# Optimization experiments

Measured on AMD Instinct MI355X. Metric: run time of the kernel, lower is better.

The kernel has to match this reference:

```python
import jax, jax.numpy as jnp
import numpy as np

B, H, W, C = 32, 56, 56, 512
WS, SHIFT, NH = 7, 3, 16
N = WS * WS
NW = (H // WS) * (W // WS)
HID = 4 * C
EPS = 1e-5


def _np_constants():
    # log-spaced relative coords table (SwinV2 CPB input), pretrained_window_size=[0,0]
    rh = np.arange(-(WS - 1), WS, dtype=np.float32)
    tbl = np.stack(np.meshgrid(rh, rh, indexing='ij'), axis=-1)  # (2*WS-1, 2*WS-1, 2)
    tbl = tbl / (WS - 1) * 8.0
    tbl = np.sign(tbl) * np.log2(np.abs(tbl) + 1.0) / np.log2(8.0)
    coords = np.stack(np.meshgrid(np.arange(WS), np.arange(WS), indexing='ij'))
    cf = coords.reshape(2, -1)
    rc = (cf[:, :, None] - cf[:, None, :]).transpose(1, 2, 0).copy()  # (N,N,2)
    rc[..., 0] += WS - 1
    rc[..., 1] += WS - 1
    rc[..., 0] *= 2 * WS - 1
    rpi = rc.sum(-1)  # (N,N) indices into the (2*WS-1)^2 table
    # shifted-window attention mask
    img = np.zeros((H, W), dtype=np.float32)
    sl = (slice(0, -WS), slice(-WS, -SHIFT), slice(-SHIFT, None))
    cnt = 0
    for hs in sl:
        for ws in sl:
            img[hs, ws] = cnt
            cnt += 1
    mw = img.reshape(H // WS, WS, W // WS, WS).transpose(0, 2, 1, 3).reshape(-1, N)
    am = mw[:, None, :] - mw[:, :, None]
    attn_mask = np.where(am != 0, -100.0, 0.0).astype(np.float32)  # (NW,N,N)
    return tbl.reshape(-1, 2).astype(np.float32), rpi.reshape(-1), attn_mask

TBL_NP, RPI_NP, MASK_NP = _np_constants()


def _ln(x, g, b):
    mu = jnp.mean(x, -1, keepdims=True)
    var = jnp.mean((x - mu) ** 2, -1, keepdims=True)
    return (x - mu) * jax.lax.rsqrt(var + EPS) * g + b


def _win_part(x):  # (B,H,W,C) -> (B*NW, N, C)
    x = x.reshape(B, H // WS, WS, W // WS, WS, C).transpose(0, 1, 3, 2, 4, 5)
    return x.reshape(-1, N, C)


def _win_rev(w):  # (B*NW, N, C) -> (B,H,W,C)
    x = w.reshape(B, H // WS, W // WS, WS, WS, C).transpose(0, 1, 3, 2, 4, 5)
    return x.reshape(B, H, W, C)


def setup_inputs() -> dict:
    key = jax.random.key(0)
    ks = jax.random.split(key, 8)
    s = 0.02
    return {
        'x': jax.random.normal(ks[0], (B, H * W, C), jnp.float32),
        'qkv_w': jax.random.normal(ks[1], (3 * C, C), jnp.float32) * s,
        'q_bias': jnp.zeros((C,), jnp.float32),
        'v_bias': jnp.zeros((C,), jnp.float32),
        'logit_scale': jnp.log(10.0) * jnp.ones((NH, 1, 1), jnp.float32),
        'cpb_w1': jax.random.normal(ks[2], (512, 2), jnp.float32) * s,
        'cpb_b1': jnp.zeros((512,), jnp.float32),
        'cpb_w2': jax.random.normal(ks[3], (NH, 512), jnp.float32) * s,
        'proj_w': jax.random.normal(ks[4], (C, C), jnp.float32) * s,
        'proj_b': jnp.zeros((C,), jnp.float32),
        'norm1_g': jnp.ones((C,), jnp.float32),
        'norm1_b': jnp.zeros((C,), jnp.float32),
        'fc1_w': jax.random.normal(ks[5], (HID, C), jnp.float32) * s,
        'fc1_b': jnp.zeros((HID,), jnp.float32),
        'fc2_w': jax.random.normal(ks[6], (C, HID), jnp.float32) * s,
        'fc2_b': jnp.zeros((C,), jnp.float32),
        'norm2_g': jnp.ones((C,), jnp.float32),
        'norm2_b': jnp.zeros((C,), jnp.float32),
    }


def reference(x, qkv_w, q_bias, v_bias, logit_scale, cpb_w1, cpb_b1, cpb_w2,
              proj_w, proj_b, norm1_g, norm1_b, fc1_w, fc1_b, fc2_w, fc2_b,
              norm2_g, norm2_b):
    tbl = jnp.asarray(TBL_NP)
    mask = jnp.asarray(MASK_NP)
    shortcut = x
    xi = x.reshape(B, H, W, C)
    xi = jnp.roll(xi, shift=(-SHIFT, -SHIFT), axis=(1, 2))
    xw = _win_part(xi)  # (B*NW, N, C)
    qkv_bias = jnp.concatenate([q_bias, jnp.zeros_like(v_bias), v_bias])
    qkv = xw @ qkv_w.T + qkv_bias
    qkv = qkv.reshape(-1, N, 3, NH, C // NH).transpose(2, 0, 3, 1, 4)
    q, k, v = qkv[0], qkv[1], qkv[2]  # (B_, NH, N, hd)
    qn = q / jnp.maximum(jnp.linalg.norm(q, axis=-1, keepdims=True), 1e-12)
    kn = k / jnp.maximum(jnp.linalg.norm(k, axis=-1, keepdims=True), 1e-12)
    scale = jnp.exp(jnp.minimum(logit_scale, jnp.log(100.0)))  # (NH,1,1)
    attn = jnp.einsum('bhnd,bhmd->bhnm', qn, kn) * scale
    # CPB MLP -> relative position bias
    hcb = jax.nn.relu(tbl @ cpb_w1.T + cpb_b1)       # (169, 512)
    bias_tbl = hcb @ cpb_w2.T                        # (169, NH)
    rpb = bias_tbl[RPI_NP].reshape(N, N, NH).transpose(2, 0, 1)
    rpb = 16.0 * jax.nn.sigmoid(rpb)
    attn = attn + rpb[None]
    attn = attn.reshape(B, NW, NH, N, N) + mask[None, :, None]
    attn = jax.nn.softmax(attn.reshape(-1, NH, N, N), axis=-1)
    out = jnp.einsum('bhnm,bhmd->bhnd', attn, v).transpose(0, 2, 1, 3).reshape(-1, N, C)
    out = out @ proj_w.T + proj_b
    xi = _win_rev(out)
    xi = jnp.roll(xi, shift=(SHIFT, SHIFT), axis=(1, 2)).reshape(B, H * W, C)
    x = shortcut + _ln(xi, norm1_g, norm1_b)  # SwinV2 post-norm residual
    hmlp = jax.nn.gelu(x @ fc1_w.T + fc1_b, approximate=False)
    m = hmlp @ fc2_w.T + fc2_b
    x = x + _ln(m, norm2_g, norm2_b)
    return x
```

## Files before the change

kernel.cpp:

```cpp
#include <hip/hip_runtime.h>

typedef unsigned short u16;
typedef unsigned int   u32;

using f32x4  = __attribute__((ext_vector_type(4))) float;
using bf16x8 = __attribute__((ext_vector_type(8))) short;

__device__ __forceinline__ float bf2f(u16 u){
  union { u32 i; float f; } x; x.i = ((u32)u) << 16; return x.f;
}
__device__ __forceinline__ u16 f2bf(float f){
  union { float f; u32 i; } x; x.f = f;
  u32 r = x.i + 0x7FFFu + ((x.i >> 16) & 1u);
  return (u16)(r >> 16);
}
__device__ __forceinline__ float gelu_f(float v){
  float u = 0.7978845608f * v * (1.f + 0.044715f*v*v);
  float e = __expf(2.f*u);
  return 0.5f*v*(2.f - 2.f/(e + 1.f));
}

__device__ __forceinline__ void glds16(const void* g, void* l){
  __builtin_amdgcn_global_load_lds(
      (const __attribute__((address_space(1))) unsigned int*)g,
      (__attribute__((address_space(3))) unsigned int*)(unsigned int)(unsigned long long)l,
      16, 0, 0);
}

__device__ __forceinline__ int rollmap(int m){
  int win = m / 49, n = m % 49;
  int b  = win >> 6, wi = win & 63;
  int wh = wi >> 3, ww = wi & 7;
  int r = n / 7, c = n % 7;
  int sh = wh*7 + r + 3; if (sh >= 56) sh -= 56;
  int sw = ww*7 + c + 3; if (sw >= 56) sw -= 56;
  return b*3136 + sh*56 + sw;
}

template<int EPI, int AMODE, int NKT>
__global__ __launch_bounds__(512, 2) void gemm_bt(const u16* __restrict__ A,
      const u16* __restrict__ Bw, const float* __restrict__ bias,
      void* __restrict__ outp, int M, int N, int nbn)
{
  constexpr int K = NKT * 64;
  __shared__ __align__(16) char LDS[2*65536];
  const int t    = threadIdx.x;
  const int lane = t & 63, wave = t >> 6;
  const int wr = wave >> 2, wn = wave & 3;
  const int lr = lane & 15, lk = lane >> 4;

  const int gl = ((blockIdx.x & 7) * ((int)gridDim.x >> 3)) + (blockIdx.x >> 3);
  const int bm = gl / nbn, bn = gl - bm*nbn;

  const int q   = (t & 7) ^ ((t >> 3) & 7);
  const int sr0 = 2*(t >> 3) + (q >> 2);
  const int sch = (q & 3) * 8;
  const u16 *pA0, *pA1;
  if constexpr (AMODE == 0){
    pA0 = A + (size_t)(bm*256 + sr0      )*K + sch;
    pA1 = A + (size_t)(bm*256 + sr0 + 128)*K + sch;
  } else {
    pA0 = A + (size_t)rollmap(bm*256 + sr0      )*K + sch;
    pA1 = A + (size_t)rollmap(bm*256 + sr0 + 128)*K + sch;
  }
  const u16* pB0 = Bw + (size_t)(bn*256 + sr0      )*K + sch;
  const u16* pB1 = Bw + (size_t)(bn*256 + sr0 + 128)*K + sch;

  int oA[8], oB[4];
#pragma unroll
  for (int i = 0; i < 8; ++i){
    int r = wr*128 + i*16 + lr;
    oA[i] = ((r>>1)<<7) + (((((r&1)<<2)|lk) ^ ((r>>1)&7))<<4);
  }
#pragma unroll
  for (int j = 0; j < 4; ++j){
    int r = wn*64 + j*16 + lr;
    oB[j] = ((r>>1)<<7) + (((((r&1)<<2)|lk) ^ ((r>>1)&7))<<4);
  }

  f32x4 acc[8][4];
#pragma unroll
  for (int i = 0; i < 8; ++i)
#pragma unroll
    for (int j = 0; j < 4; ++j) acc[i][j] = (f32x4){0.f, 0.f, 0.f, 0.f};

  auto stgA = [&](int T, int ks, int buf){
    char* d = LDS + buf*65536 + ks*16384 + wave*1024;
    const int e = T*64 + ks*32;
    glds16(pA0 + e, d);
    glds16(pA1 + e, d + 8192);
  };
  auto stgB = [&](int T, int ks, int buf){
    char* d = LDS + buf*65536 + 32768 + ks*16384 + wave*1024;
    const int e = T*64 + ks*32;
    glds16(pB0 + e, d);
    glds16(pB1 + e, d + 8192);
  };

  stgA(0,0,0); stgA(0,1,0); stgB(0,0,0); stgB(0,1,0);
  stgA(1,0,1); stgA(1,1,1); stgB(1,0,1); stgB(1,1,1);
  asm volatile("s_waitcnt vmcnt(8)" ::: "memory");
  __builtin_amdgcn_s_barrier();
  asm volatile("" ::: "memory");

  auto TILE = [&](int T, int buf){
    const char* ld = LDS + buf*65536;
    const bool stP0  = (T >= 1) && (T+1 < NKT);
    const bool st123 = (T+2 < NKT);
    bf16x8 fa[4], fb[4];

#pragma unroll
    for (int j = 0; j < 4; ++j) fb[j] = *(const bf16x8*)(ld + 32768 + oB[j]);
#pragma unroll
    for (int i = 0; i < 4; ++i) fa[i] = *(const bf16x8*)(ld + oA[i]);
    if (stP0) stgA(T+1, 1, buf^1);
    __builtin_amdgcn_s_barrier();
    asm volatile("s_waitcnt lgkmcnt(0)" ::: "memory");
    __builtin_amdgcn_sched_barrier(0);
    __builtin_amdgcn_s_setprio(1);
#pragma unroll
    for (int i = 0; i < 4; ++i)
#pragma unroll
      for (int j = 0; j < 4; ++j)
        acc[i][j] = __builtin_amdgcn_mfma_f32_16x16x32_bf16(fa[i], fb[j], acc[i][j], 0, 0, 0);
    __builtin_amdgcn_s_setprio(0);
    __builtin_amdgcn_s_barrier();
    asm volatile("" ::: "memory");

#pragma unroll
    for (int i = 0; i < 4; ++i) fa[i] = *(const bf16x8*)(ld + oA[4+i]);
    if (st123) stgB(T+2, 0, buf);
    __builtin_amdgcn_s_barrier();
    asm volatile("s_waitcnt lgkmcnt(0)" ::: "memory");
    __builtin_amdgcn_sched_barrier(0);
    __builtin_amdgcn_s_setprio(1);
#pragma unroll
    for (int i = 0; i < 4; ++i)
#pragma unroll
      for (int j = 0; j < 4; ++j)
        acc[4+i][j] = __builtin_amdgcn_mfma_f32_16x16x32_bf16(fa[i], fb[j], acc[4+i][j], 0, 0, 0);
    __builtin_amdgcn_s_setprio(0);
    __builtin_amdgcn_s_barrier();
    asm volatile("" ::: "memory");

#pragma unroll
    for (int j = 0; j < 4; ++j) fb[j] = *(const bf16x8*)(ld + 49152 + oB[j]);
#pragma unroll
    for (int i = 0; i < 4; ++i) fa[i] = *(const bf16x8*)(ld + 16384 + oA[i]);
    if (st123) stgA(T+2, 0, buf);
    __builtin_amdgcn_s_barrier();
    asm volatile("s_waitcnt lgkmcnt(0)" ::: "memory");
    __builtin_amdgcn_sched_barrier(0);
    __builtin_amdgcn_s_setprio(1);
#pragma unroll
    for (int i = 0; i < 4; ++i)
#pragma unroll
      for (int j = 0; j < 4; ++j)
        acc[i][j] = __builtin_amdgcn_mfma_f32_16x16x32_bf16(fa[i], fb[j], acc[i][j], 0, 0, 0);
    __builtin_amdgcn_s_setprio(0);
    __builtin_amdgcn_s_barrier();
    asm volatile("" ::: "memory");

#pragma unroll
    for (int i = 0; i < 4; ++i) fa[i] = *(const bf16x8*)(ld + 16384 + oA[4+i]);
    if (st123) stgB(T+2, 1, buf);
    __builtin_amdgcn_s_barrier();
    asm volatile("s_waitcnt lgkmcnt(0)" ::: "memory");
    __builtin_amdgcn_sched_barrier(0);
    __builtin_amdgcn_s_setprio(1);
#pragma unroll
    for (int i = 0; i < 4; ++i)
#pragma unroll
      for (int j = 0; j < 4; ++j)
        acc[4+i][j] = __builtin_amdgcn_mfma_f32_16x16x32_bf16(fa[i], fb[j], acc[4+i][j], 0, 0, 0);
    __builtin_amdgcn_s_setprio(0);
    if (T <= NKT-3)      asm volatile("s_waitcnt vmcnt(6)" ::: "memory");
    else if (T == NKT-2) asm volatile("s_waitcnt vmcnt(0)" ::: "memory");
    if (T < NKT-1){
      __builtin_amdgcn_s_barrier();
      asm volatile("" ::: "memory");
    }
  };

  for (int p = 0; p < NKT/2; ++p){
    TILE(2*p,     0);
    TILE(2*p + 1, 1);
  }

  const int lc = lane & 15, lg = lane >> 4;
#pragma unroll
  for (int i = 0; i < 8; ++i){
#pragma unroll
    for (int j = 0; j < 4; ++j){
      int cm = bm*256 + wr*128 + i*16 + lg*4;
      int cn = bn*256 + wn*64  + j*16 + lc;
      float bv = bias[cn];
#pragma unroll
      for (int r = 0; r < 4; ++r){
        float v = acc[i][j][r] + bv;
        if (EPI == 2) v = gelu_f(v);
        ((u16*)outp)[(size_t)(cm + r)*N + cn] = f2bf(v);
      }
    }
  }
}

__global__ __launch_bounds__(256, 2) void attn_mfma(const u16* __restrict__ qkv,
      const float* __restrict__ rpb, const float* __restrict__ ls,
      u16* __restrict__ outp)
{
  __shared__ __align__(16) u16 Pl[4][64*72];
  __shared__ __align__(16) u16 Vl[4][32*72];
  __shared__ unsigned char regid[64];
  const int tid  = threadIdx.x, lane = tid & 63, wave = tid >> 6;
  const int lc = lane & 15, lg = lane >> 4;
  const int pair = blockIdx.x*4 + wave;
  const int win = pair >> 4, h = pair & 15;

  const u16* qb = qkv + (size_t)win*49*1536 + h*32;
  const u16* kb = qb + 512;
  const u16* vb = qb + 1024;

  if (tid < 49){
    int wi = win & 63, wh = wi >> 3, ww = wi & 7;
    int q7 = (tid*37) >> 8, r7 = tid - q7*7;
    int gh = wh*7 + q7, gw = ww*7 + r7;
    int rh = gh < 49 ? 0 : (gh < 53 ? 1 : 2);
    int rw = gw < 49 ? 0 : (gw < 53 ? 1 : 2);
    regid[tid] = (unsigned char)(rh*3 + rw);
  }

  u16* V = &Vl[wave][0];
#pragma unroll
  for (int it = 0; it < 4; ++it){
    int ch = it*64 + lane;
    int n = ch >> 2, oct = ch & 3;
    union { int4 i4; u16 s[8]; } v8;
    if (n < 49) v8.i4 = *(const int4*)(vb + (size_t)n*1536 + oct*8);
    else        v8.i4 = make_int4(0,0,0,0);
#pragma unroll
    for (int q = 0; q < 8; ++q) V[(oct*8 + q)*72 + n] = v8.s[q];
  }

  const float scale = __expf(fminf(ls[h], 4.6051702f));
  bf16x8 qf[4], kf[4];
#pragma unroll
  for (int ti = 0; ti < 4; ++ti){
    const int n = ti*16 + lc;
    {
      union { int4 i4; u16 s[8]; } raw;
      raw.i4 = *(const int4*)(qb + (size_t)n*1536 + lg*8);
      float f[8]; float ss = 0.f;
#pragma unroll
      for (int q = 0; q < 8; ++q){ f[q] = bf2f(raw.s[q]); ss += f[q]*f[q]; }
      ss += __shfl_xor(ss, 16); ss += __shfl_xor(ss, 32);
      const float inv = scale / fmaxf(sqrtf(ss), 1e-12f);
      union { short s[8]; bf16x8 v; } o;
#pragma unroll
      for (int q = 0; q < 8; ++q) o.s[q] = (short)f2bf(f[q]*inv);
      qf[ti] = o.v;
    }
    {
      union { int4 i4; u16 s[8]; } raw;
      raw.i4 = *(const int4*)(kb + (size_t)n*1536 + lg*8);
      float f[8]; float ss = 0.f;
#pragma unroll
      for (int q = 0; q < 8; ++q){ f[q] = bf2f(raw.s[q]); ss += f[q]*f[q]; }
      ss += __shfl_xor(ss, 16); ss += __shfl_xor(ss, 32);
      const float inv = 1.f / fmaxf(sqrtf(ss), 1e-12f);
      union { short s[8]; bf16x8 v; } o;
#pragma unroll
      for (int q = 0; q < 8; ++q) o.s[q] = (short)f2bf(f[q]*inv);
      kf[ti] = o.v;
    }
  }
  __syncthreads();

  f32x4 acc[4][4];
#pragma unroll
  for (int i = 0; i < 4; ++i)
#pragma unroll
    for (int j = 0; j < 4; ++j) acc[i][j] = (f32x4){0.f,0.f,0.f,0.f};
#pragma unroll
  for (int i = 0; i < 4; ++i)
#pragma unroll
    for (int j = 0; j < 4; ++j)
      acc[i][j] = __builtin_amdgcn_mfma_f32_16x16x32_bf16(qf[i], kf[j], acc[i][j], 0, 0, 0);

  u16* P = &Pl[wave][0];
  int rj[4];
#pragma unroll
  for (int tj = 0; tj < 4; ++tj){
    int j = tj*16 + lc;
    rj[tj] = (int)regid[j < 49 ? j : 0];
  }
  const float* rpbh = rpb + h*2401;
#pragma unroll
  for (int ti = 0; ti < 4; ++ti){
#pragma unroll
    for (int r = 0; r < 4; ++r){
      const int i = ti*16 + lg*4 + r;
      const bool iv = i < 49;
      const int ic = iv ? i : 0;
      const int ri = (int)regid[ic];
      const float* rrow = rpbh + ic*49;
      float sv[4];
#pragma unroll
      for (int tj = 0; tj < 4; ++tj){
        const int j = tj*16 + lc;
        float t2 = acc[ti][tj][r] + rrow[j < 49 ? j : 0];
        if (ri != rj[tj]) t2 -= 100.f;
        sv[tj] = (iv && j < 49) ? t2 : -1e30f;
      }
      float mx = fmaxf(fmaxf(sv[0],sv[1]), fmaxf(sv[2],sv[3]));
      mx = fmaxf(mx, __shfl_xor(mx, 1));
      mx = fmaxf(mx, __shfl_xor(mx, 2));
      mx = fmaxf(mx, __shfl_xor(mx, 4));
      mx = fmaxf(mx, __shfl_xor(mx, 8));
      float p[4], sum = 0.f;
#pragma unroll
      for (int tj = 0; tj < 4; ++tj){ p[tj] = __expf(sv[tj] - mx); sum += p[tj]; }
      sum += __shfl_xor(sum, 1); sum += __shfl_xor(sum, 2);
      sum += __shfl_xor(sum, 4); sum += __shfl_xor(sum, 8);
      const float rs = __builtin_amdgcn_rcpf(sum);
#pragma unroll
      for (int tj = 0; tj < 4; ++tj) P[i*72 + tj*16 + lc] = f2bf(p[tj]*rs);
    }
  }
  __syncthreads();

  f32x4 o[4][2];
#pragma unroll
  for (int i = 0; i < 4; ++i){ o[i][0] = (f32x4){0.f,0.f,0.f,0.f}; o[i][1] = (f32x4){0.f,0.f,0.f,0.f}; }
#pragma unroll
  for (int ks = 0; ks < 2; ++ks){
    bf16x8 pa[4], vf[2];
#pragma unroll
    for (int ti = 0; ti < 4; ++ti)
      pa[ti] = *(const bf16x8*)((const char*)P + (ti*16 + lc)*144 + (ks*4 + lg)*16);
#pragma unroll
    for (int tc = 0; tc < 2; ++tc)
      vf[tc] = *(const bf16x8*)((const char*)V + (tc*16 + lc)*144 + (ks*4 + lg)*16);
#pragma unroll
    for (int ti = 0; ti < 4; ++ti)
#pragma unroll
      for (int tc = 0; tc < 2; ++tc)
        o[ti][tc] = __builtin_amdgcn_mfma_f32_16x16x32_bf16(pa[ti], vf[tc], o[ti][tc], 0, 0, 0);
  }

#pragma unroll
  for (int ti = 0; ti < 4; ++ti){
#pragma unroll
    for (int tc = 0; tc < 2; ++tc){
#pragma unroll
      for (int r = 0; r < 4; ++r){
        const int i = ti*16 + lg*4 + r;
        if (i < 49)
          outp[((size_t)win*49 + i)*512 + h*32 + tc*16 + lc] = f2bf(o[ti][tc][r]);
      }
    }
  }
}

__global__ __launch_bounds__(256) void ln1_kernel(const u16* __restrict__ xb,
      const u16* __restrict__ y, const float* __restrict__ g, const float* __restrict__ bt,
      float* __restrict__ xout, u16* __restrict__ xbf)
{
  __shared__ float red[8];
  const int t = blockIdx.x;
  const int b = t / 3136, s = t % 3136;
  const int hh = s / 56, ww2 = s % 56;
  int ph = hh + 53; if (ph >= 56) ph -= 56;
  int pw = ww2 + 53; if (pw >= 56) pw -= 56;
  const int win = b*64 + (ph/7)*8 + (pw/7);
  const int n   = (ph%7)*7 + (pw%7);
  const u16* yr = y + ((size_t)win*49 + n)*512;
  const int c = threadIdx.x * 2;
  u32 u = *(const u32*)(yr + c);
  float vx = bf2f((u16)(u & 0xffff)), vy = bf2f((u16)(u >> 16));
  float sum = vx + vy, sq = vx*vx + vy*vy;
#pragma unroll
  for (int off = 32; off; off >>= 1){ sum += __shfl_xor(sum, off); sq += __shfl_xor(sq, off); }
  if ((threadIdx.x & 63) == 0){ red[threadIdx.x >> 6] = sum; red[(threadIdx.x >> 6) + 4] = sq; }
  __syncthreads();
  sum = red[0]+red[1]+red[2]+red[3];
  sq  = red[4]+red[5]+red[6]+red[7];
  const float mu  = sum * (1.f/512.f);
  const float inv = rsqrtf(fmaxf(sq * (1.f/512.f) - mu*mu, 0.f) + 1e-5f);
  u32 ux = *(const u32*)(xb + (size_t)t*512 + c);
  float o0 = bf2f((u16)(ux & 0xffff)) + (vx - mu)*inv*g[c]   + bt[c];
  float o1 = bf2f((u16)(ux >> 16))    + (vy - mu)*inv*g[c+1] + bt[c+1];
  float* orow = xout + (size_t)t*512;
  orow[c] = o0; orow[c+1] = o1;
  *(u32*)(xbf + (size_t)t*512 + c) = (u32)f2bf(o0) | ((u32)f2bf(o1) << 16);
}

__global__ __launch_bounds__(256) void ln2_kernel(const u16* __restrict__ m,
      const float* __restrict__ g, const float* __restrict__ bt, float* __restrict__ out)
{
  __shared__ float red[8];
  const int t = blockIdx.x;
  const int c = threadIdx.x * 2;
  u32 u = *(const u32*)(m + (size_t)t*512 + c);
  float v0 = bf2f((u16)(u & 0xffff)), v1 = bf2f((u16)(u >> 16));
  float sum = v0 + v1, sq = v0*v0 + v1*v1;
#pragma unroll
  for (int off = 32; off; off >>= 1){ sum += __shfl_xor(sum, off); sq += __shfl_xor(sq, off); }
  if ((threadIdx.x & 63) == 0){ red[threadIdx.x >> 6] = sum; red[(threadIdx.x >> 6) + 4] = sq; }
  __syncthreads();
  sum = red[0]+red[1]+red[2]+red[3];
  sq  = red[4]+red[5]+red[6]+red[7];
  const float mu  = sum * (1.f/512.f);
  const float inv = rsqrtf(fmaxf(sq * (1.f/512.f) - mu*mu, 0.f) + 1e-5f);
  float* orow = out + (size_t)t*512;
  orow[c]   += (v0 - mu)*inv*g[c]   + bt[c];
  orow[c+1] += (v1 - mu)*inv*g[c+1] + bt[c+1];
}

__global__ void cast_bf16_kernel(const float* __restrict__ in, u16* __restrict__ out, int n4){
  int i = blockIdx.x*256 + threadIdx.x;
  if (i >= n4) return;
  float4 v = *(const float4*)(in + (size_t)i*4);
  u32 lo = (u32)f2bf(v.x) | ((u32)f2bf(v.y) << 16);
  u32 hi = (u32)f2bf(v.z) | ((u32)f2bf(v.w) << 16);
  *(uint2*)(out + (size_t)i*4) = make_uint2(lo, hi);
}
__global__ void qkvbias_kernel(const float* __restrict__ qb, const float* __restrict__ vb,
                               float* __restrict__ out){
  int i = blockIdx.x*256 + threadIdx.x;
  if (i >= 1536) return;
  out[i] = i < 512 ? qb[i] : (i < 1024 ? 0.f : vb[i - 1024]);
}
__device__ __forceinline__ float cpb_coord(int d){
  float v = (float)(d - 6) * (8.f/6.f);
  float m = log2f(fabsf(v) + 1.f) * (1.f/3.f);
  return v > 0.f ? m : (v < 0.f ? -m : 0.f);
}
__global__ void cpb_kernel(const float* __restrict__ w1, const float* __restrict__ b1,
                           const float* __restrict__ w2, float* __restrict__ btbl){
  int idx = blockIdx.x*256 + threadIdx.x;
  if (idx >= 169*16) return;
  int e = idx >> 4, h = idx & 15;
  float t0 = cpb_coord(e / 13), t1 = cpb_coord(e % 13);
  float acc = 0.f;
  for (int jj = 0; jj < 512; ++jj){
    float hid = fmaxf(t0*w1[jj*2] + t1*w1[jj*2+1] + b1[jj], 0.f);
    acc += hid * w2[h*512 + jj];
  }
  btbl[e*16 + h] = acc;
}
__global__ void rpb_kernel(const float* __restrict__ btbl, float* __restrict__ rpb){
  int idx = blockIdx.x*256 + threadIdx.x;
  if (idx >= 16*49*49) return;
  int hh = idx / 2401, ij = idx % 2401, i = ij / 49, j = ij % 49;
  int dr = i/7 - j/7 + 6, dc = i%7 - j%7 + 6;
  float bb = btbl[(dr*13 + dc)*16 + hh];
  rpb[idx] = 16.f / (1.f + __expf(-bb));
}

extern "C" void kernel_launch(void* const* d_in, const int* in_sizes, int n_in,
                              void* d_out, int out_size, void* d_ws, size_t ws_size,
                              hipStream_t stream)
{
  const float* x    = (const float*)d_in[0];
  const float* qkvw = (const float*)d_in[1];
  const float* qb   = (const float*)d_in[2];
  const float* vb   = (const float*)d_in[3];
  const float* ls   = (const float*)d_in[4];
  const float* cw1  = (const float*)d_in[5];
  const float* cb1  = (const float*)d_in[6];
  const float* cw2  = (const float*)d_in[7];
  const float* pw   = (const float*)d_in[8];
  const float* pb   = (const float*)d_in[9];
  const float* n1g  = (const float*)d_in[10];
  const float* n1b  = (const float*)d_in[11];
  const float* f1w  = (const float*)d_in[12];
  const float* f1b  = (const float*)d_in[13];
  const float* f2w  = (const float*)d_in[14];
  const float* f2b  = (const float*)d_in[15];
  const float* n2g  = (const float*)d_in[16];
  const float* n2b  = (const float*)d_in[17];

  char* ws = (char*)d_ws;
  const size_t SZ_BIG = (size_t)100352 * 2048 * 2;
  const size_t SZ_MID = (size_t)100352 * 512  * 2;
  size_t o = SZ_BIG + SZ_MID;
  u16* wqkv  = (u16*)(ws + o); o += (size_t)1536*512*2;
  u16* wproj = (u16*)(ws + o); o += (size_t)512*512*2;
  u16* wfc1  = (u16*)(ws + o); o += (size_t)2048*512*2;
  u16* wfc2  = (u16*)(ws + o); o += (size_t)512*2048*2;
  float* qkvbias = (float*)(ws + o); o += 1536*4;
  float* btbl    = (float*)(ws + o); o += 2704*4;
  float* rpb     = (float*)(ws + o); o += 38416*4;

  u16*   xbf   = (u16*)ws;
  u16*   qkvo  = (u16*)(ws + (size_t)100352*512*2);
  u16*   y_h   = qkvo;
  u16*   big_h = (u16*)ws;
  u16*   mid   = (u16*)(ws + SZ_BIG);
  float* out   = (float*)d_out;

  cast_bf16_kernel<<<768,  256, 0, stream>>>(qkvw, wqkv, 1536*512/4);
  cast_bf16_kernel<<<256,  256, 0, stream>>>(pw,  wproj, 512*512/4);
  cast_bf16_kernel<<<1024, 256, 0, stream>>>(f1w, wfc1, 2048*512/4);
  cast_bf16_kernel<<<1024, 256, 0, stream>>>(f2w, wfc2, 512*2048/4);
  qkvbias_kernel<<<6, 256, 0, stream>>>(qb, vb, qkvbias);
  cpb_kernel<<<11, 256, 0, stream>>>(cw1, cb1, cw2, btbl);
  rpb_kernel<<<151, 256, 0, stream>>>(btbl, rpb);
  cast_bf16_kernel<<<50176, 256, 0, stream>>>(x, xbf, 100352*512/4);

  gemm_bt<0,2,8><<<392*6, 512, 0, stream>>>(xbf, wqkv, qkvbias,
                                            (void*)qkvo, 100352, 1536, 6);
  attn_mfma<<<8192, 256, 0, stream>>>(qkvo, rpb, ls, mid);
  gemm_bt<0,0,8><<<392*2, 512, 0, stream>>>(mid, wproj, pb,
                                            (void*)y_h, 100352, 512, 2);
  ln1_kernel<<<100352, 256, 0, stream>>>(xbf, y_h, n1g, n1b, out, mid);
  gemm_bt<2,0,8><<<392*8, 512, 0, stream>>>(mid, wfc1, f1b,
                                            (void*)big_h, 100352, 2048, 8);
  gemm_bt<0,0,32><<<392*2, 512, 0, stream>>>(big_h, wfc2, f2b,
                                             (void*)mid, 100352, 512, 2);
  ln2_kernel<<<100352, 256, 0, stream>>>(mid, n2g, n2b, out);
}
```

Baseline: 1.454 ms.

## Shrink GEMM K-tile to 32 with simple double-buffered loop

Restructures the bf16 GEMM main loop so each step processes a 32-wide K slab instead of a 64-wide tile split into two half-stages. It uses a plain two-buffer ping-pong that prefetches only the next slab, and drops the vmcnt(6) deep-prefetch scheme along with most intra-tile barriers. LDS drops to 64 KB, which could raise occupancy, and the launch-bounds hint for two blocks per CU is removed. In exchange the loop now waits on vmcnt(0) every iteration, so each slab's global load latency is less well hidden.

Result: slower. 1.525 ms (median of 3 runs) (+4.9%).

```diff
diff --git a/kernel.cpp b/kernel.cpp
--- a/kernel.cpp
+++ b/kernel.cpp
@@ -38,12 +38,12 @@
 }
 
 template<int EPI, int AMODE, int NKT>
-__global__ __launch_bounds__(512, 2) void gemm_bt(const u16* __restrict__ A,
+__global__ __launch_bounds__(512) void gemm_bt(const u16* __restrict__ A,
       const u16* __restrict__ Bw, const float* __restrict__ bias,
       void* __restrict__ outp, int M, int N, int nbn)
 {
-  constexpr int K = NKT * 64;
-  __shared__ __align__(16) char LDS[2*65536];
+  constexpr int K = NKT * 32;
+  __shared__ __align__(16) char LDS[2*32768];
   const int t    = threadIdx.x;
   const int lane = t & 63, wave = t >> 6;
   const int wr = wave >> 2, wn = wave & 3;
@@ -84,37 +84,34 @@
 #pragma unroll
     for (int j = 0; j < 4; ++j) acc[i][j] = (f32x4){0.f, 0.f, 0.f, 0.f};
 
-  auto stgA = [&](int T, int ks, int buf){
-    char* d = LDS + buf*65536 + ks*16384 + wave*1024;
-    const int e = T*64 + ks*32;
+  auto stgA = [&](int T, int buf){
+    char* d = LDS + buf*32768 + wave*1024;
+    const int e = T*32;
     glds16(pA0 + e, d);
     glds16(pA1 + e, d + 8192);
   };
-  auto stgB = [&](int T, int ks, int buf){
-    char* d = LDS + buf*65536 + 32768 + ks*16384 + wave*1024;
-    const int e = T*64 + ks*32;
+  auto stgB = [&](int T, int buf){
+    char* d = LDS + buf*32768 + 16384 + wave*1024;
+    const int e = T*32;
     glds16(pB0 + e, d);
     glds16(pB1 + e, d + 8192);
   };
 
-  stgA(0,0,0); stgA(0,1,0); stgB(0,0,0); stgB(0,1,0);
-  stgA(1,0,1); stgA(1,1,1); stgB(1,0,1); stgB(1,1,1);
-  asm volatile("s_waitcnt vmcnt(8)" ::: "memory");
+  stgA(0, 0); stgB(0, 0);
+  asm volatile("s_waitcnt vmcnt(0)" ::: "memory");
   __builtin_amdgcn_s_barrier();
   asm volatile("" ::: "memory");
 
-  auto TILE = [&](int T, int buf){
-    const char* ld = LDS + buf*65536;
-    const bool stP0  = (T >= 1) && (T+1 < NKT);
-    const bool st123 = (T+2 < NKT);
+  for (int T = 0; T < NKT; ++T){
+    const char* ld = LDS + (T & 1)*32768;
+    const int nb = (T & 1) ^ 1;
     bf16x8 fa[4], fb[4];
 
-#pragma unroll
-    for (int j = 0; j < 4; ++j) fb[j] = *(const bf16x8*)(ld + 32768 + oB[j]);
+    if (T + 1 < NKT) stgA(T + 1, nb);
+#pragma unroll
+    for (int j = 0; j < 4; ++j) fb[j] = *(const bf16x8*)(ld + 16384 + oB[j]);
 #pragma unroll
     for (int i = 0; i < 4; ++i) fa[i] = *(const bf16x8*)(ld + oA[i]);
-    if (stP0) stgA(T+1, 1, buf^1);
-    __builtin_amdgcn_s_barrier();
     asm volatile("s_waitcnt lgkmcnt(0)" ::: "memory");
     __builtin_amdgcn_sched_barrier(0);
     __builtin_amdgcn_s_setprio(1);
@@ -124,13 +121,10 @@
       for (int j = 0; j < 4; ++j)
         acc[i][j] = __builtin_amdgcn_mfma_f32_16x16x32_bf16(fa[i], fb[j], acc[i][j], 0, 0, 0);
     __builtin_amdgcn_s_setprio(0);
-    __builtin_amdgcn_s_barrier();
-    asm volatile("" ::: "memory");
-
+
+    if (T + 1 < NKT) stgB(T + 1, nb);
 #pragma unroll
     for (int i = 0; i < 4; ++i) fa[i] = *(const bf16x8*)(ld + oA[4+i]);
-    if (st123) stgB(T+2, 0, buf);
-    __builtin_amdgcn_s_barrier();
     asm volatile("s_waitcnt lgkmcnt(0)" ::: "memory");
     __builtin_amdgcn_sched_barrier(0);
     __builtin_amdgcn_s_setprio(1);
@@ -140,51 +134,12 @@
       for (int j = 0; j < 4; ++j)
         acc[4+i][j] = __builtin_amdgcn_mfma_f32_16x16x32_bf16(fa[i], fb[j], acc[4+i][j], 0, 0, 0);
     __builtin_amdgcn_s_setprio(0);
-    __builtin_amdgcn_s_barrier();
-    asm volatile("" ::: "memory");
-
-#pragma unroll
-    for (int j = 0; j < 4; ++j) fb[j] = *(const bf16x8*)(ld + 49152 + oB[j]);
-#pragma unroll
-    for (int i = 0; i < 4; ++i) fa[i] = *(const bf16x8*)(ld + 16384 + oA[i]);
-    if (st123) stgA(T+2, 0, buf);
-    __builtin_amdgcn_s_barrier();
-    asm volatile("s_waitcnt lgkmcnt(0)" ::: "memory");
-    __builtin_amdgcn_sched_barrier(0);
-    __builtin_amdgcn_s_setprio(1);
-#pragma unroll
-    for (int i = 0; i < 4; ++i)
-#pragma unroll
-      for (int j = 0; j < 4; ++j)
-        acc[i][j] = __builtin_amdgcn_mfma_f32_16x16x32_bf16(fa[i], fb[j], acc[i][j], 0, 0, 0);
-    __builtin_amdgcn_s_setprio(0);
-    __builtin_amdgcn_s_barrier();
-    asm volatile("" ::: "memory");
-
-#pragma unroll
-    for (int i = 0; i < 4; ++i) fa[i] = *(const bf16x8*)(ld + 16384 + oA[4+i]);
-    if (st123) stgB(T+2, 1, buf);
-    __builtin_amdgcn_s_barrier();
-    asm volatile("s_waitcnt lgkmcnt(0)" ::: "memory");
-    __builtin_amdgcn_sched_barrier(0);
-    __builtin_amdgcn_s_setprio(1);
-#pragma unroll
-    for (int i = 0; i < 4; ++i)
-#pragma unroll
-      for (int j = 0; j < 4; ++j)
-        acc[4+i][j] = __builtin_amdgcn_mfma_f32_16x16x32_bf16(fa[i], fb[j], acc[4+i][j], 0, 0, 0);
-    __builtin_amdgcn_s_setprio(0);
-    if (T <= NKT-3)      asm volatile("s_waitcnt vmcnt(6)" ::: "memory");
-    else if (T == NKT-2) asm volatile("s_waitcnt vmcnt(0)" ::: "memory");
-    if (T < NKT-1){
+
+    if (T + 1 < NKT){
+      asm volatile("s_waitcnt vmcnt(0)" ::: "memory");
       __builtin_amdgcn_s_barrier();
       asm volatile("" ::: "memory");
     }
-  };
-
-  for (int p = 0; p < NKT/2; ++p){
-    TILE(2*p,     0);
-    TILE(2*p + 1, 1);
   }
 
   const int lc = lane & 15, lg = lane >> 4;
@@ -509,15 +464,15 @@
   rpb_kernel<<<151, 256, 0, stream>>>(btbl, rpb);
   cast_bf16_kernel<<<50176, 256, 0, stream>>>(x, xbf, 100352*512/4);
 
-  gemm_bt<0,2,8><<<392*6, 512, 0, stream>>>(xbf, wqkv, qkvbias,
-                                            (void*)qkvo, 100352, 1536, 6);
+  gemm_bt<0,2,16><<<392*6, 512, 0, stream>>>(xbf, wqkv, qkvbias,
+                                             (void*)qkvo, 100352, 1536, 6);
   attn_mfma<<<8192, 256, 0, stream>>>(qkvo, rpb, ls, mid);
-  gemm_bt<0,0,8><<<392*2, 512, 0, stream>>>(mid, wproj, pb,
-                                            (void*)y_h, 100352, 512, 2);
+  gemm_bt<0,0,16><<<392*2, 512, 0, stream>>>(mid, wproj, pb,
+                                             (void*)y_h, 100352, 512, 2);
   ln1_kernel<<<100352, 256, 0, stream>>>(xbf, y_h, n1g, n1b, out, mid);
-  gemm_bt<2,0,8><<<392*8, 512, 0, stream>>>(mid, wfc1, f1b,
-                                            (void*)big_h, 100352, 2048, 8);
-  gemm_bt<0,0,32><<<392*2, 512, 0, stream>>>(big_h, wfc2, f2b,
+  gemm_bt<2,0,16><<<392*8, 512, 0, stream>>>(mid, wfc1, f1b,
+                                             (void*)big_h, 100352, 2048, 8);
+  gemm_bt<0,0,64><<<392*2, 512, 0, stream>>>(big_h, wfc2, f2b,
                                              (void*)mid, 100352, 512, 2);
   ln2_kernel<<<100352, 256, 0, stream>>>(mid, n2g, n2b, out);
 }
```

## Fuse fc1+GELU, fc2 and LayerNorm2 residual into one MLP kernel

Applied to the files above, without the earlier changes.

Replaces the fc1 GEMM, fc2 GEMM and ln2 kernel with a single kernel. Each block owns 128 rows and loops over 8 hidden chunks of 256. For each chunk it computes fc1 with GELU into LDS, then accumulates the fc2 product in registers, and finishes with a fused LayerNorm and residual add. This avoids writing and re-reading the large 2048-wide bf16 hidden activation and drops the separate LN pass. In exchange, every block re-streams both full weight matrices. The GEMM pipeline is simpler: one 32-wide K step at a time, synchronised per step, with 128 KB of LDS limiting occupancy.

After: 2.147 ms. 1.48x slower.

```diff
diff --git a/kernel.cpp b/kernel.cpp
--- a/kernel.cpp
+++ b/kernel.cpp
@@ -13,6 +13,9 @@
   union { float f; u32 i; } x; x.f = f;
   u32 r = x.i + 0x7FFFu + ((x.i >> 16) & 1u);
   return (u16)(r >> 16);
+}
+__device__ __forceinline__ u32 pack2(float a, float b){
+  return (u32)f2bf(a) | ((u32)f2bf(b) << 16);
 }
 __device__ __forceinline__ float gelu_f(float v){
   float u = 0.7978845608f * v * (1.f + 0.044715f*v*v);
@@ -35,6 +38,10 @@
   int sh = wh*7 + r + 3; if (sh >= 56) sh -= 56;
   int sw = ww*7 + c + 3; if (sw >= 56) sw -= 56;
   return b*3136 + sh*56 + sw;
+}
+
+__device__ __forceinline__ int rowswz(int r, int ck){
+  return ((r>>1)<<7) + (((((r&1)<<2)|ck) ^ ((r>>1)&7))<<4);
 }
 
 template<int EPI, int AMODE, int NKT>
@@ -68,15 +75,9 @@
 
   int oA[8], oB[4];
 #pragma unroll
-  for (int i = 0; i < 8; ++i){
-    int r = wr*128 + i*16 + lr;
-    oA[i] = ((r>>1)<<7) + (((((r&1)<<2)|lk) ^ ((r>>1)&7))<<4);
-  }
-#pragma unroll
-  for (int j = 0; j < 4; ++j){
-    int r = wn*64 + j*16 + lr;
-    oB[j] = ((r>>1)<<7) + (((((r&1)<<2)|lk) ^ ((r>>1)&7))<<4);
-  }
+  for (int i = 0; i < 8; ++i) oA[i] = rowswz(wr*128 + i*16 + lr, lk);
+#pragma unroll
+  for (int j = 0; j < 4; ++j) oB[j] = rowswz(wn*64 + j*16 + lr, lk);
 
   f32x4 acc[8][4];
 #pragma unroll
@@ -200,6 +201,184 @@
         float v = acc[i][j][r] + bv;
         if (EPI == 2) v = gelu_f(v);
         ((u16*)outp)[(size_t)(cm + r)*N + cn] = f2bf(v);
+      }
+    }
+  }
+}
+
+__global__ __launch_bounds__(512, 2) void fused_mlp(const u16* __restrict__ X,
+      const u16* __restrict__ W1, const float* __restrict__ f1b,
+      const u16* __restrict__ W2, const float* __restrict__ f2b,
+      const float* __restrict__ g2, const float* __restrict__ bt2,
+      float* __restrict__ out)
+{
+  __shared__ __align__(16) char LDS[131072];
+  const int t = threadIdx.x, lane = t & 63, wave = t >> 6;
+  const int lr = lane & 15, lk = lane >> 4;
+  const int bm = ((blockIdx.x & 7) * ((int)gridDim.x >> 3)) + (blockIdx.x >> 3);
+
+  const int q   = (t & 7) ^ ((t >> 3) & 7);
+  const int sr0 = 2*(t >> 3) + (q >> 2);
+  const int sch = (q & 3) * 8;
+  const u16* pX  = X  + (size_t)(bm*128 + sr0)*512 + sch;
+  const u16* pW1 = W1 + (size_t)sr0*512 + sch;
+  const u16* pW2 = W2 + (size_t)sr0*2048 + sch;
+
+  const int wr1 = wave >> 1, wn1 = wave & 1;
+  int o1A[4], o1B[4];
+#pragma unroll
+  for (int i = 0; i < 4; ++i) o1A[i] = rowswz(wr1*64 + i*16 + lr, lk);
+#pragma unroll
+  for (int j = 0; j < 4; ++j) o1B[j] = rowswz(wn1*64 + j*16 + lr, lk);
+  const int wr2 = wave >> 2, wn2 = wave & 3;
+  int o2B[8], mr_[4];
+#pragma unroll
+  for (int j = 0; j < 8; ++j) o2B[j] = rowswz(wn2*128 + j*16 + lr, lk);
+#pragma unroll
+  for (int i = 0; i < 4; ++i) mr_[i] = wr2*64 + i*16 + lr;
+
+  auto stage1 = [&](int hc, int kt, int buf){
+    char* d = LDS + 65536 + buf*24576;
+    const u16* w = pW1 + (size_t)(hc*256)*512 + kt*32;
+    glds16(w,                   d +         wave*1024);
+    glds16(w + (size_t)128*512, d +  8192 + wave*1024);
+    glds16(pX + kt*32,          d + 16384 + wave*1024);
+  };
+  auto stage2 = [&](int hc, int kt, int buf){
+    char* d = LDS + 65536 + buf*32768;
+    const u16* w = pW2 + hc*256 + kt*32;
+    glds16(w,                    d +         wave*1024);
+    glds16(w + (size_t)128*2048, d +  8192 + wave*1024);
+    glds16(w + (size_t)256*2048, d + 16384 + wave*1024);
+    glds16(w + (size_t)384*2048, d + 24576 + wave*1024);
+  };
+
+  f32x4 acc2[4][8];
+#pragma unroll
+  for (int i = 0; i < 4; ++i)
+#pragma unroll
+    for (int j = 0; j < 8; ++j) acc2[i][j] = (f32x4){0.f,0.f,0.f,0.f};
+
+  for (int hc = 0; hc < 8; ++hc){
+    float4 b1v[4];
+#pragma unroll
+    for (int i = 0; i < 4; ++i)
+      b1v[i] = *(const float4*)(f1b + hc*256 + wr1*64 + i*16 + lk*4);
+
+    f32x4 acc1[4][4];
+#pragma unroll
+    for (int i = 0; i < 4; ++i)
+#pragma unroll
+      for (int j = 0; j < 4; ++j) acc1[i][j] = (f32x4){0.f,0.f,0.f,0.f};
+
+    stage1(hc, 0, 0);
+    __syncthreads();
+    for (int kt = 0; kt < 16; ++kt){
+      const char* ld = LDS + 65536 + (kt & 1)*24576;
+      if (kt + 1 < 16) stage1(hc, kt + 1, (kt & 1) ^ 1);
+      bf16x8 fa[4], fb[4];
+#pragma unroll
+      for (int i = 0; i < 4; ++i) fa[i] = *(const bf16x8*)(ld + o1A[i]);
+#pragma unroll
+      for (int j = 0; j < 4; ++j) fb[j] = *(const bf16x8*)(ld + 16384 + o1B[j]);
+      asm volatile("s_waitcnt lgkmcnt(0)" ::: "memory");
+      __builtin_amdgcn_sched_barrier(0);
+      __builtin_amdgcn_s_setprio(1);
+#pragma unroll
+      for (int i = 0; i < 4; ++i)
+#pragma unroll
+        for (int j = 0; j < 4; ++j)
+          acc1[i][j] = __builtin_amdgcn_mfma_f32_16x16x32_bf16(fa[i], fb[j], acc1[i][j], 0, 0, 0);
+      __builtin_amdgcn_s_setprio(0);
+      __syncthreads();
+    }
+
+#pragma unroll
+    for (int i = 0; i < 4; ++i){
+      const float* bp = (const float*)&b1v[i];
+#pragma unroll
+      for (int j = 0; j < 4; ++j){
+        float g0 = gelu_f(acc1[i][j][0] + bp[0]);
+        float g1 = gelu_f(acc1[i][j][1] + bp[1]);
+        float g2_ = gelu_f(acc1[i][j][2] + bp[2]);
+        float g3 = gelu_f(acc1[i][j][3] + bp[3]);
+        int m = wn1*64 + j*16 + lr;
+        int u = wr1*8 + i*2 + (lk >> 1);
+        char* p = LDS + m*512 + ((u ^ (m & 7)) << 4) + ((lk & 1) << 3);
+        uint2 w2v; w2v.x = pack2(g0, g1); w2v.y = pack2(g2_, g3);
+        *(uint2*)p = w2v;
+      }
+    }
+    __syncthreads();
+
+    stage2(hc, 0, 0);
+    __syncthreads();
+    for (int kt = 0; kt < 8; ++kt){
+      const char* ld = LDS + 65536 + (kt & 1)*32768;
+      if (kt + 1 < 8) stage2(hc, kt + 1, (kt & 1) ^ 1);
+      bf16x8 fa[4], fb[8];
+#pragma unroll
+      for (int i = 0; i < 4; ++i)
+        fa[i] = *(const bf16x8*)(LDS + mr_[i]*512 + (((kt*4 + lk) ^ (mr_[i] & 7)) << 4));
+#pragma unroll
+      for (int j = 0; j < 8; ++j) fb[j] = *(const bf16x8*)(ld + o2B[j]);
+      asm volatile("s_waitcnt lgkmcnt(0)" ::: "memory");
+      __builtin_amdgcn_sched_barrier(0);
+      __builtin_amdgcn_s_setprio(1);
+#pragma unroll
+      for (int i = 0; i < 4; ++i)
+#pragma unroll
+        for (int j = 0; j < 8; ++j)
+          acc2[i][j] = __builtin_amdgcn_mfma_f32_16x16x32_bf16(fa[i], fb[j], acc2[i][j], 0, 0, 0);
+      __builtin_amdgcn_s_setprio(0);
+      __syncthreads();
+    }
+  }
+
+  float g2v[8], btv[8], fbv[8];
+#pragma unroll
+  for (int j = 0; j < 8; ++j){
+    int cn = wn2*128 + j*16 + lr;
+    g2v[j] = g2[cn]; btv[j] = bt2[cn]; fbv[j] = f2b[cn];
+  }
+  float* scr = (float*)(LDS + 65536);
+#pragma unroll
+  for (int i = 0; i < 4; ++i){
+#pragma unroll
+    for (int r = 0; r < 4; ++r){
+      float s = 0.f, ss = 0.f;
+#pragma unroll
+      for (int j = 0; j < 8; ++j){
+        float v = acc2[i][j][r] + fbv[j];
+        s += v; ss += v*v;
+      }
+      s  += __shfl_xor(s, 1);  s  += __shfl_xor(s, 2);
+      s  += __shfl_xor(s, 4);  s  += __shfl_xor(s, 8);
+      ss += __shfl_xor(ss, 1); ss += __shfl_xor(ss, 2);
+      ss += __shfl_xor(ss, 4); ss += __shfl_xor(ss, 8);
+      if (lr == 0){
+        int row = wr2*64 + i*16 + lk*4 + r;
+        scr[(row*4 + wn2)*2]     = s;
+        scr[(row*4 + wn2)*2 + 1] = ss;
+      }
+    }
+  }
+  __syncthreads();
+#pragma unroll
+  for (int i = 0; i < 4; ++i){
+#pragma unroll
+    for (int r = 0; r < 4; ++r){
+      int row = wr2*64 + i*16 + lk*4 + r;
+      float s  = scr[row*8+0] + scr[row*8+2] + scr[row*8+4] + scr[row*8+6];
+      float ss = scr[row*8+1] + scr[row*8+3] + scr[row*8+5] + scr[row*8+7];
+      float mu  = s * (1.f/512.f);
+      float inv = rsqrtf(fmaxf(ss * (1.f/512.f) - mu*mu, 0.f) + 1e-5f);
+      float* orow = out + (size_t)(bm*128 + row)*512;
+#pragma unroll
+      for (int j = 0; j < 8; ++j){
+        int cn = wn2*128 + j*16 + lr;
+        float v = acc2[i][j][r] + fbv[j];
+        orow[cn] += (v - mu)*inv*g2v[j] + btv[j];
       }
     }
   }
@@ -393,28 +572,6 @@
   float* orow = xout + (size_t)t*512;
   orow[c] = o0; orow[c+1] = o1;
   *(u32*)(xbf + (size_t)t*512 + c) = (u32)f2bf(o0) | ((u32)f2bf(o1) << 16);
-}
-
-__global__ __launch_bounds__(256) void ln2_kernel(const u16* __restrict__ m,
-      const float* __restrict__ g, const float* __restrict__ bt, float* __restrict__ out)
-{
-  __shared__ float red[8];
-  const int t = blockIdx.x;
-  const int c = threadIdx.x * 2;
-  u32 u = *(const u32*)(m + (size_t)t*512 + c);
-  float v0 = bf2f((u16)(u & 0xffff)), v1 = bf2f((u16)(u >> 16));
-  float sum = v0 + v1, sq = v0*v0 + v1*v1;
-#pragma unroll
-  for (int off = 32; off; off >>= 1){ sum += __shfl_xor(sum, off); sq += __shfl_xor(sq, off); }
-  if ((threadIdx.x & 63) == 0){ red[threadIdx.x >> 6] = sum; red[(threadIdx.x >> 6) + 4] = sq; }
-  __syncthreads();
-  sum = red[0]+red[1]+red[2]+red[3];
-  sq  = red[4]+red[5]+red[6]+red[7];
-  const float mu  = sum * (1.f/512.f);
-  const float inv = rsqrtf(fmaxf(sq * (1.f/512.f) - mu*mu, 0.f) + 1e-5f);
-  float* orow = out + (size_t)t*512;
-  orow[c]   += (v0 - mu)*inv*g[c]   + bt[c];
-  orow[c+1] += (v1 - mu)*inv*g[c+1] + bt[c+1];
 }
 
 __global__ void cast_bf16_kernel(const float* __restrict__ in, u16* __restrict__ out, int n4){
@@ -496,7 +653,6 @@
   u16*   xbf   = (u16*)ws;
   u16*   qkvo  = (u16*)(ws + (size_t)100352*512*2);
   u16*   y_h   = qkvo;
-  u16*   big_h = (u16*)ws;
   u16*   mid   = (u16*)(ws + SZ_BIG);
   float* out   = (float*)d_out;
 
@@ -515,9 +671,5 @@
   gemm_bt<0,0,8><<<392*2, 512, 0, stream>>>(mid, wproj, pb,
                                             (void*)y_h, 100352, 512, 2);
   ln1_kernel<<<100352, 256, 0, stream>>>(xbf, y_h, n1g, n1b, out, mid);
-  gemm_bt<2,0,8><<<392*8, 512, 0, stream>>>(mid, wfc1, f1b,
-                                            (void*)big_h, 100352, 2048, 8);
-  gemm_bt<0,0,32><<<392*2, 512, 0, stream>>>(big_h, wfc2, f2b,
-                                             (void*)mid, 100352, 512, 2);
-  ln2_kernel<<<100352, 256, 0, stream>>>(mid, n2g, n2b, out);
-}
+  fused_mlp<<<784, 512, 0, stream>>>(mid, wfc1, f1b, wfc2, f2b, n2g, n2b, out);
+}
```
